# Performance work log

Hardware: AMD Instinct MI355X
Metric: run time of the kernel (lower is better)

Reference implementation:

```python
import jax, jax.numpy as jnp
import numpy as np

K = 3
OFFSET_SCALE = 0.25
GN_GROUPS = 8
GN_EPS = 1e-5


def setup_inputs() -> dict:
    key = jax.random.key(0)
    k1, k2, k3 = jax.random.split(key, 3)
    N, C, H, W = 4, 128, 96, 96
    Cout = 128
    x = jax.random.normal(k1, (N, C, H, W), dtype=jnp.float32)
    # offset head: small random weights so offsets are modest (tanh tames anyway)
    w_head = jax.random.normal(k2, (3, C, 3, 3), dtype=jnp.float32) * 0.05
    b_head = jnp.zeros((3,), dtype=jnp.float32)
    # kaiming-ish scale for the deform conv weight: sqrt(2 / fan_out)
    w_dcn = jax.random.normal(k3, (Cout, C, 3, 3), dtype=jnp.float32) * np.sqrt(2.0 / (Cout * 9))
    gn_gamma = jnp.ones((Cout,), dtype=jnp.float32)
    gn_beta = jnp.zeros((Cout,), dtype=jnp.float32)
    return {"x": x, "w_head": w_head, "b_head": b_head, "w_dcn": w_dcn,
            "gn_gamma": gn_gamma, "gn_beta": gn_beta}


def _conv3x3(x, w, b):
    y = jax.lax.conv_general_dilated(
        x, w, window_strides=(1, 1), padding=((1, 1), (1, 1)),
        dimension_numbers=("NCHW", "OIHW", "NCHW"))
    return y + b[None, :, None, None]


def _deform_sample(xn, py, px):
    # xn: (C,H,W); py/px: (9,H,W) absolute sampling coords (y=row, x=col)
    C, H, W = xn.shape
    y0 = jnp.floor(py).astype(jnp.int32)
    x0 = jnp.floor(px).astype(jnp.int32)
    fy = py - y0
    fx = px - x0
    xf = xn.reshape(C, H * W)

    def corner(yi, xi, wgt):
        valid = (yi >= 0) & (yi < H) & (xi >= 0) & (xi < W)
        idx = jnp.clip(yi, 0, H - 1) * W + jnp.clip(xi, 0, W - 1)  # (9,H,W)
        v = xf[:, idx.reshape(-1)].reshape(C, *idx.shape)  # (C,9,H,W)
        return v * (wgt * valid)[None]

    return (corner(y0, x0, (1 - fy) * (1 - fx))
            + corner(y0, x0 + 1, (1 - fy) * fx)
            + corner(y0 + 1, x0, fy * (1 - fx))
            + corner(y0 + 1, x0 + 1, fy * fx))


def reference(x, w_head, b_head, w_dcn, gn_gamma, gn_beta):
    N, C, H, W = x.shape
    Cout = w_dcn.shape[0]
    stride, pad, dil = 1, 1, 1

    head = _conv3x3(x, w_head, b_head)                 # (N,3,H,W)
    dx, dy, m = head[:, :1], head[:, 1:2], head[:, 2:3]
    mask = jax.nn.sigmoid(m)                           # (N,1,H,W) broadcast over 9 taps
    dx = OFFSET_SCALE * jnp.tanh(dx)
    dy = OFFSET_SCALE * jnp.tanh(dy)

    # serpentine 18-channel offsets, mmcv layout: (oy, ox) pairs per kernel tap
    z = jnp.zeros_like(dx)
    offs = jnp.concatenate(
        [z, z, z, dy, z, -dy, dx, z, z, z, -dx, z, dx, dy, dx, -dy, -dx, dy], axis=1)
    offs = offs.reshape(N, 9, 2, H, W)
    oy, ox = offs[:, :, 0], offs[:, :, 1]              # (N,9,H,W)

    ky = jnp.arange(9) // 3
    kx = jnp.arange(9) % 3
    base_y = (jnp.arange(H) * stride - pad)[None, :, None] + (ky * dil)[:, None, None]
    base_x = (jnp.arange(W) * stride - pad)[None, None, :] + (kx * dil)[:, None, None]
    py = base_y[None] + oy                             # (N,9,H,W)
    px = base_x[None] + ox

    sampled = jax.vmap(_deform_sample)(x, py, px)      # (N,C,9,H,W)
    sampled = sampled * mask[:, None]                  # modulated

    y = jnp.einsum('nckhw,ock->nohw', sampled, w_dcn.reshape(Cout, C, 9))

    # GroupNorm(8, Cout) + ReLU
    G = min(GN_GROUPS, Cout)
    yg = y.reshape(N, G, Cout // G, H, W)
    mu = yg.mean(axis=(2, 3, 4), keepdims=True)
    var = yg.var(axis=(2, 3, 4), keepdims=True)
    yn = ((yg - mu) * jax.lax.rsqrt(var + GN_EPS)).reshape(N, Cout, H, W)
    yn = yn * gn_gamma[None, :, None, None] + gn_beta[None, :, None, None]
    return jax.nn.relu(yn)
```

## Files before the change

kernel.cpp:

```cpp
#include <hip/hip_runtime.h>
#include <hip/hip_bf16.h>
#include <math.h>

#define NB   4
#define CIN  128
#define HH   96
#define WW   96
#define HWN  (HH*WW)
#define NHW  (NB*HWN)
#define COUT 128
#define KW   9
#define KDIM (CIN*KW)
#define GSZ  16
#define PXB  32
#define NBLK (NHW/PXB)
#define XPB  64

typedef __attribute__((ext_vector_type(8))) short bf16x8;
typedef __attribute__((ext_vector_type(4))) float f32x4;

#define OFF_WAH   0
#define OFF_DX    147456
#define OFF_DY    184320
#define OFF_MASK  221184
#define OFF_GN    258048
#define OFF_MAP   258240
#define OFF_PAIR  258496
#define OFF_XT    258560

#define HEADB 1152

__device__ __forceinline__ ushort f2bf(float f) {
    union { float f; uint u; } v; v.f = f;
    uint r = v.u + 0x7fffu + ((v.u >> 16) & 1u);
    return (ushort)(r >> 16);
}

__device__ __forceinline__ void barrier_keep_vm() {
    asm volatile("s_waitcnt lgkmcnt(0)\n\ts_barrier" ::: "memory");
}

__global__ __launch_bounds__(256) void pre_kernel(const float* __restrict__ x,
                                                  const float* __restrict__ w_head,
                                                  const float* __restrict__ b_head,
                                                  const float* __restrict__ wd,
                                                  ushort* __restrict__ wah,
                                                  float* __restrict__ dxv,
                                                  float* __restrict__ dyv,
                                                  float* __restrict__ maskv,
                                                  float* __restrict__ gn_part,
                                                  int* __restrict__ map,
                                                  int* __restrict__ pairB) {
    __shared__ float wl[CIN * 28];
    __shared__ float sp[32][8][13];
    const int b = blockIdx.x, t = threadIdx.x;

    if (b >= HEADB) {
        const int bb = b - HEADB;
        int i = bb * 256 + t;
        {
            int e  = i & 7;
            int l  = (i >> 3) & 63;
            int ot = (i >> 9) & 7;
            int q  = (i >> 12) & 3;
            int k  = i >> 14;
            int o  = ot * 16 + (l & 15);
            int c  = q * 32 + (l >> 4) * 8 + e;
            wah[i] = f2bf(wd[o * KDIM + c * KW + k]);
        }
        if (bb == 0 && t < 128) gn_part[t] = 0.f;
        if (bb == 0 && t < 64) {
            int l = t;
            bf16x8 A1 = {}, B1 = {}, A2 = {}, B2 = {};
            if ((l >> 4) == 0) {
                A1[0] = (short)f2bf((float)((l & 15) + 1));
                B1[0] = (short)f2bf(1.0f);
                A2[0] = (short)f2bf(1.0f);
                B2[0] = (short)f2bf((float)((l & 15) + 1));
            }
            f32x4 d1 = {0.f,0.f,0.f,0.f}, d2 = {0.f,0.f,0.f,0.f};
            d1 = __builtin_amdgcn_mfma_f32_16x16x32_bf16(A1, B1, d1, 0, 0, 0);
            d2 = __builtin_amdgcn_mfma_f32_16x16x32_bf16(A2, B2, d2, 0, 0, 0);
#pragma unroll
            for (int r = 0; r < 4; ++r) {
                int m = (int)(d1[r] + 0.5f) - 1;
                int n = (int)(d2[r] + 0.5f) - 1;
                map[l * 4 + r] = (m << 4) | n;
            }
        }
        if (bb == 1 && t < 64) {
            int l = t;
            union { bf16x8 v; short a[8]; } B;
#pragma unroll
            for (int e = 0; e < 8; ++e) {
                float val = (float)(1u << (((l >> 4) * 8 + e) & 31));
                B.a[e] = (short)f2bf(val);
            }
#pragma unroll
            for (int s = 0; s < 32; ++s) {
                union { bf16x8 v; short a[8]; } A;
#pragma unroll
                for (int e = 0; e < 8; ++e) A.a[e] = 0;
                if ((l >> 4) == (s >> 3)) A.a[s & 7] = (short)f2bf(1.0f);
                f32x4 d = {0.f, 0.f, 0.f, 0.f};
                d = __builtin_amdgcn_mfma_f32_16x16x32_bf16(A.v, B.v, d, 0, 0, 0);
                float v0 = d[0];
                if (l == 0 && v0 > 0.f) {
                    int ex; frexpf(v0, &ex);
                    int j = ex - 1;
                    if (j >= 0 && j < 32) pairB[j] = s;
                }
            }
        }
        return;
    }

    for (int i = t; i < 3456; i += 256) {
        int j = i / KDIM, r = i - j * KDIM;
        int c = r / 9, kk = r - c * 9;
        wl[c * 28 + kk * 3 + j] = w_head[i];
    }
    __syncthreads();

    const int sl = t & 7;
    const int cg = t >> 3;
    const int p0 = b * 32 + sl * 4;
    const int n  = p0 / HWN;
    const int hw = p0 - n * HWN;
    const int h  = hw / WW;
    const int w0 = hw - h * WW;
    const float* xn = x + (size_t)n * CIN * HWN;
    const bool lok = (w0 > 0);
    const bool rok = (w0 < WW - 4);

    float acc[12];
#pragma unroll
    for (int i = 0; i < 12; ++i) acc[i] = 0.f;

#pragma unroll
    for (int cc = 0; cc < 4; ++cc) {
        const int c = cg * 4 + cc;
        const float* xc = xn + (size_t)c * HWN;
        float v[3][6];
#pragma unroll
        for (int r = 0; r < 3; ++r) {
            int y = h - 1 + r;
            if (y >= 0 && y < HH) {
                const float* xr = xc + y * WW + w0;
                float4 m4 = *(const float4*)xr;
                v[r][1] = m4.x; v[r][2] = m4.y; v[r][3] = m4.z; v[r][4] = m4.w;
                v[r][0] = lok ? xr[-1] : 0.f;
                v[r][5] = rok ? xr[4]  : 0.f;
            } else {
#pragma unroll
                for (int i = 0; i < 6; ++i) v[r][i] = 0.f;
            }
        }
        float wr[28];
        const float* wc = &wl[c * 28];
#pragma unroll
        for (int i2 = 0; i2 < 7; ++i2) {
            float4 q4 = *(const float4*)(wc + i2 * 4);
            wr[i2 * 4 + 0] = q4.x; wr[i2 * 4 + 1] = q4.y;
            wr[i2 * 4 + 2] = q4.z; wr[i2 * 4 + 3] = q4.w;
        }
#pragma unroll
        for (int ky = 0; ky < 3; ++ky)
#pragma unroll
            for (int kx = 0; kx < 3; ++kx) {
                const int kk = ky * 3 + kx;
                const float wj0 = wr[kk * 3 + 0];
                const float wj1 = wr[kk * 3 + 1];
                const float wj2 = wr[kk * 3 + 2];
#pragma unroll
                for (int q = 0; q < 4; ++q) {
                    float val = v[ky][q + kx];
                    acc[q * 3 + 0] = fmaf(val, wj0, acc[q * 3 + 0]);
                    acc[q * 3 + 1] = fmaf(val, wj1, acc[q * 3 + 1]);
                    acc[q * 3 + 2] = fmaf(val, wj2, acc[q * 3 + 2]);
                }
            }
    }
#pragma unroll
    for (int i = 0; i < 12; ++i) sp[cg][sl][i] = acc[i];
    __syncthreads();
    if (cg < 8) {
#pragma unroll
        for (int k = 8; k < 32; k += 8)
#pragma unroll
            for (int i = 0; i < 12; ++i) sp[cg][sl][i] += sp[cg + k][sl][i];
    }
    __syncthreads();
    if (t < 32) {
        const int s2 = t >> 2, q = t & 3;
        float b0 = b_head[0], b1 = b_head[1], b2 = b_head[2];
#pragma unroll
        for (int cgi = 0; cgi < 8; ++cgi) {
            b0 += sp[cgi][s2][q * 3 + 0];
            b1 += sp[cgi][s2][q * 3 + 1];
            b2 += sp[cgi][s2][q * 3 + 2];
        }
        int pp = b * 32 + t;
        dxv[pp]   = 0.25f * tanhf(b0);
        dyv[pp]   = 0.25f * tanhf(b1);
        maskv[pp] = 1.f / (1.f + expf(-b2));
    }
}

__global__ __launch_bounds__(256) void xpose_kernel(const float* __restrict__ x,
                                                    const int* __restrict__ pairB,
                                                    float* __restrict__ xt) {
    __shared__ float tile[CIN][XPB + 1];
    __shared__ int sperm[CIN];
    const int b = blockIdx.x, t = threadIdx.x;
    const int p0 = b * XPB;
    const int n  = p0 / HWN, hw0 = p0 % HWN;
    const float* xn = x + (size_t)n * CIN * HWN + hw0;

    if (t < CIN) {
        int q = t >> 5, j = t & 31;
        sperm[t] = q * 32 + (pairB[j] & 31);
    }
    __syncthreads();

#pragma unroll
    for (int rep = 0; rep < 4; ++rep) {
        const int c  = rep * 32 + (t >> 3);
        const int px = (t & 7) * 8;
        const float* src = xn + (size_t)c * HWN + px;
        float4 a = *(const float4*)src;
        float4 bq = *(const float4*)(src + 4);
        tile[c][px + 0] = a.x;  tile[c][px + 1] = a.y;
        tile[c][px + 2] = a.z;  tile[c][px + 3] = a.w;
        tile[c][px + 4] = bq.x; tile[c][px + 5] = bq.y;
        tile[c][px + 6] = bq.z; tile[c][px + 7] = bq.w;
    }
    __syncthreads();

    const int px = t >> 2, jg = t & 3;
    float* dst = xt + ((size_t)p0 + px) * CIN + jg * 32;
#pragma unroll
    for (int jj = 0; jj < 32; jj += 4) {
        float4 v;
        v.x = tile[sperm[jg * 32 + jj + 0]][px];
        v.y = tile[sperm[jg * 32 + jj + 1]][px];
        v.z = tile[sperm[jg * 32 + jj + 2]][px];
        v.w = tile[sperm[jg * 32 + jj + 3]][px];
        *(float4*)(dst + jj) = v;
    }
}

__global__ __launch_bounds__(256) void dcn_kernel(const float* __restrict__ xt,
                                                  const ushort* __restrict__ wah,
                                                  const float* __restrict__ dxv,
                                                  const float* __restrict__ dyv,
                                                  const float* __restrict__ maskv,
                                                  const int* __restrict__ map,
                                                  float* __restrict__ out,
                                                  float* __restrict__ gn_part) {
    __shared__ __attribute__((aligned(16))) ushort sBh[2][4 * PXB * 8];
    __shared__ float sMask[PXB];
    __shared__ float gred[16];

    const int t = threadIdx.x;
    const int lane = t & 63;
    const int wv = t >> 6;
    const int lg = lane >> 4;
    const int ml = lane & 15;
    const int pix = t & 31;
    const int sg  = t >> 5;

    int b = blockIdx.x;
    int nb = (b & 7) * (NBLK / 8) + (b >> 3);
    const int p0  = nb * PXB;
    const int n   = p0 / HWN;
    const int hw0 = p0 % HWN;
    const float* xtn = xt + (size_t)n * HWN * CIN;

    if (t < PXB) sMask[t] = maskv[p0 + t];
    if (t < 16) gred[t] = 0.f;

    const float dxl = dxv[p0 + pix];
    const float dyl = dyv[p0 + pix];
    const int hme = (hw0 + pix) / WW;
    const int wme = (hw0 + pix) % WW;

    f32x4 acc[2][2];
#pragma unroll
    for (int i = 0; i < 2; i++)
#pragma unroll
        for (int j = 0; j < 2; j++) acc[i][j] = (f32x4){0.f, 0.f, 0.f, 0.f};

    const int oyc[9] = {0, 0, 0, 1, 0, -1, 1, 1, -1};
    const int oxc[9] = {0, 1, -1, 0, 0, 0, 1, -1, 1};
    const int ncl[9] = {1, 2, 2, 2, 1, 2, 4, 4, 4};

    int aa[4]; float wq[4];
    float4 vr0, vr1, vr2, vr3;
    bf16x8 An0, An1;

    {
        float py = (float)(hme - 1), px = (float)(wme - 1);
        float fy0 = floorf(py), fx0 = floorf(px);
        int y0 = (int)fy0, x0 = (int)fx0;
        float fy = py - fy0, fx = px - fx0;
#pragma unroll
        for (int j = 0; j < 4; ++j) {
            int yy = y0 + (j >> 1), xx = x0 + (j & 1);
            float wb = ((j >> 1) ? fy : 1.f - fy) * ((j & 1) ? fx : 1.f - fx);
            bool ok = (yy >= 0) && (yy < HH) && (xx >= 0) && (xx < WW);
            aa[j] = min(max(yy, 0), HH - 1) * WW + min(max(xx, 0), WW - 1);
            wq[j] = ok ? wb : 0.f;
        }
        vr0 = *(const float4*)(xtn + ((aa[0] << 7) + sg * 4));
        const size_t abase = (size_t)(wv * 2) * 512 + lane * 8;
        An0 = *(const bf16x8*)(wah + abase);
        An1 = *(const bf16x8*)(wah + abase + 512);
    }

#pragma unroll
    for (int j = 0; j < 36; ++j) {
        const int k = j >> 2;
        const int NC = ncl[k];
        bf16x8 Ah0 = An0, Ah1 = An1;
        union { short4 v; ushort u[4]; } hv;
        {
            float s0 = vr0.x * wq[0], s1 = vr0.y * wq[0];
            float s2 = vr0.z * wq[0], s3 = vr0.w * wq[0];
            if (NC >= 2) {
                s0 = fmaf(vr1.x, wq[1], s0); s1 = fmaf(vr1.y, wq[1], s1);
                s2 = fmaf(vr1.z, wq[1], s2); s3 = fmaf(vr1.w, wq[1], s3);
            }
            if (NC == 4) {
                s0 = fmaf(vr2.x, wq[2], s0); s1 = fmaf(vr2.y, wq[2], s1);
                s2 = fmaf(vr2.z, wq[2], s2); s3 = fmaf(vr2.w, wq[2], s3);
                s0 = fmaf(vr3.x, wq[3], s0); s1 = fmaf(vr3.y, wq[3], s1);
                s2 = fmaf(vr3.z, wq[3], s2); s3 = fmaf(vr3.w, wq[3], s3);
            }
            hv.u[0] = f2bf(s0); hv.u[1] = f2bf(s1);
            hv.u[2] = f2bf(s2); hv.u[3] = f2bf(s3);
        }
        const int wbase = ((sg >> 1) * PXB + pix) * 8 + (sg & 1) * 4;
        *(short4*)&sBh[j & 1][wbase] = hv.v;
        if (j < 35) {
            const int jn = j + 1, kn = jn >> 2, qn = jn & 3;
            if (qn == 0) {
                const int ky = kn / 3, kx = kn - ky * 3;
                float py = (float)(hme - 1 + ky) + (float)oyc[kn] * dxl;
                float px = (float)(wme - 1 + kx) + (float)oxc[kn] * dyl;
                float fy0 = floorf(py), fx0 = floorf(px);
                int y0 = (int)fy0, x0 = (int)fx0;
                float fy = py - fy0, fx = px - fx0;
#pragma unroll
                for (int jj = 0; jj < 4; ++jj) {
                    int yy = y0 + (jj >> 1), xx = x0 + (jj & 1);
                    float wb = ((jj >> 1) ? fy : 1.f - fy) * ((jj & 1) ? fx : 1.f - fx);
                    bool ok = (yy >= 0) && (yy < HH) && (xx >= 0) && (xx < WW);
                    aa[jj] = min(max(yy, 0), HH - 1) * WW + min(max(xx, 0), WW - 1);
                    wq[jj] = ok ? wb : 0.f;
                }
                if (ncl[kn] == 2 && oxc[kn] == 0) { aa[1] = aa[2]; wq[1] = wq[2]; }
            }
            const int NCn = ncl[kn];
            const int co = qn * 32 + sg * 4;
            vr0 = *(const float4*)(xtn + ((aa[0] << 7) + co));
            if (NCn >= 2) vr1 = *(const float4*)(xtn + ((aa[1] << 7) + co));
            if (NCn == 4) {
                vr2 = *(const float4*)(xtn + ((aa[2] << 7) + co));
                vr3 = *(const float4*)(xtn + ((aa[3] << 7) + co));
            }
            const size_t abase = (size_t)((kn * 4 + qn) * 8 + wv * 2) * 512 + lane * 8;
            An0 = *(const bf16x8*)(wah + abase);
            An1 = *(const bf16x8*)(wah + abase + 512);
        }
        barrier_keep_vm();
#pragma unroll
        for (int pt = 0; pt < 2; ++pt) {
            const int rbase = (lg * PXB + pt * 16 + ml) * 8;
            bf16x8 Bh = *(const bf16x8*)&sBh[j & 1][rbase];
            acc[0][pt] = __builtin_amdgcn_mfma_f32_16x16x32_bf16(Ah0, Bh, acc[0][pt], 0, 0, 0);
            acc[1][pt] = __builtin_amdgcn_mfma_f32_16x16x32_bf16(Ah1, Bh, acc[1][pt], 0, 0, 0);
        }
    }

    int4 mn4 = *(const int4*)&map[lane * 4];
    int mn[4] = {mn4.x, mn4.y, mn4.z, mn4.w};
    float s1g[2] = {0.f, 0.f}, s2g[2] = {0.f, 0.f};
#pragma unroll
    for (int ot = 0; ot < 2; ++ot) {
        int otile = wv * 32 + ot * 16;
#pragma unroll
        for (int pt = 0; pt < 2; ++pt) {
#pragma unroll
            for (int r = 0; r < 4; ++r) {
                int m = mn[r] >> 4, nn2 = mn[r] & 15;
                int p = pt * 16 + nn2;
                float v = acc[ot][pt][r] * sMask[p];
                s1g[ot] += v;
                s2g[ot] += v * v;
                out[((size_t)n * COUT + otile + m) * HWN + hw0 + p] = v;
            }
        }
    }
#pragma unroll
    for (int ot = 0; ot < 2; ++ot) {
        int g = wv * 2 + ot;
        atomicAdd(&gred[g * 2 + 0], s1g[ot]);
        atomicAdd(&gred[g * 2 + 1], s2g[ot]);
    }
    __syncthreads();
    if (t < 8) {
        atomicAdd(&gn_part[n * 8 + t],      gred[t * 2 + 0]);
        atomicAdd(&gn_part[64 + n * 8 + t], gred[t * 2 + 1]);
    }
}

__global__ __launch_bounds__(256) void gn_apply(float* __restrict__ out,
                                                const float* __restrict__ gn_part,
                                                const float* __restrict__ gamma,
                                                const float* __restrict__ beta) {
    int i4 = blockIdx.x * 256 + threadIdx.x;
    size_t e = (size_t)i4 * 4;
    int og = (int)(e / HWN);
    int n = og >> 7, o = og & 127;
    int s = n * 8 + (o >> 4);
    const float cnt = (float)GSZ * (float)HWN;
    float s1 = gn_part[s], s2 = gn_part[64 + s];
    float mu = s1 / cnt;
    float var = s2 / cnt - mu * mu;
    float inv = rsqrtf(var + 1e-5f);
    float ga = gamma[o] * inv;
    float be = beta[o] - mu * ga;
    float4 v = *(float4*)(out + e);
    v.x = fmaxf(fmaf(v.x, ga, be), 0.f);
    v.y = fmaxf(fmaf(v.y, ga, be), 0.f);
    v.z = fmaxf(fmaf(v.z, ga, be), 0.f);
    v.w = fmaxf(fmaf(v.w, ga, be), 0.f);
    *(float4*)(out + e) = v;
}

extern "C" void kernel_launch(void* const* d_in, const int* in_sizes, int n_in,
                              void* d_out, int out_size, void* d_ws, size_t ws_size,
                              hipStream_t stream) {
    const float* x       = (const float*)d_in[0];
    const float* w_head  = (const float*)d_in[1];
    const float* b_head  = (const float*)d_in[2];
    const float* w_dcn   = (const float*)d_in[3];
    const float* gamma   = (const float*)d_in[4];
    const float* beta    = (const float*)d_in[5];
    float* out = (float*)d_out;
    float* ws  = (float*)d_ws;

    ushort* wah    = (ushort*)(ws + OFF_WAH);
    float* dxv     = ws + OFF_DX;
    float* dyv     = ws + OFF_DY;
    float* maskv   = ws + OFF_MASK;
    float* gn_part = ws + OFF_GN;
    int*   map     = (int*)(ws + OFF_MAP);
    int*   pairB   = (int*)(ws + OFF_PAIR);
    float* xt      = ws + OFF_XT;

    pre_kernel<<<HEADB + 576, 256, 0, stream>>>(x, w_head, b_head, w_dcn, wah,
                                                dxv, dyv, maskv, gn_part, map, pairB);
    xpose_kernel<<<NHW / XPB, 256, 0, stream>>>(x, pairB, xt);
    dcn_kernel<<<NBLK, 256, 0, stream>>>(xt, wah, dxv, dyv, maskv, map, out, gn_part);
    gn_apply<<<(NB * COUT * HWN) / 4 / 256, 256, 0, stream>>>(out, gn_part, gamma, beta);
}
```

Before: 194.3 us.

## Fuse transpose kernel into pre-kernel and remap dcn thread-to-pixel layout

Folds the x transpose/permute work into the pre_kernel launch as extra blocks, each of which recomputes the MFMA lane permutation locally instead of reading pairB from global memory. This removes one kernel launch and the dependency on pairB between kernels. Shared memory becomes one union buffer sized for the largest role. It also changes the transpose store pattern to row-contiguous float4 writes and swaps the pixel/subgroup thread mapping in dcn_kernel. That mapping swap changes how sampled x rows are gathered and could affect coalescing either way.

```diff
diff --git a/kernel.cpp b/kernel.cpp
--- a/kernel.cpp
+++ b/kernel.cpp
@@ -15,6 +15,7 @@
 #define PXB  32
 #define NBLK (NHW/PXB)
 #define XPB  64
+#define XPOB (NHW/XPB)
 
 typedef __attribute__((ext_vector_type(8))) short bf16x8;
 typedef __attribute__((ext_vector_type(4))) float f32x4;
@@ -50,10 +51,76 @@
                                                   float* __restrict__ maskv,
                                                   float* __restrict__ gn_part,
                                                   int* __restrict__ map,
-                                                  int* __restrict__ pairB) {
-    __shared__ float wl[CIN * 28];
-    __shared__ float sp[32][8][13];
+                                                  int* __restrict__ pairB,
+                                                  float* __restrict__ xt) {
+    __shared__ __attribute__((aligned(16))) float smem[8480];
     const int b = blockIdx.x, t = threadIdx.x;
+
+    if (b >= HEADB + 576) {
+        float (*tile)[XPB + 1] = (float (*)[XPB + 1])smem;
+        int* sperm = (int*)(smem + CIN * (XPB + 1));
+        int* spair = (int*)(smem + CIN * (XPB + 1) + CIN);
+        const int bb2 = b - (HEADB + 576);
+        const int p0 = bb2 * XPB;
+        const int n  = p0 / HWN, hw0 = p0 % HWN;
+        const float* xn = x + (size_t)n * CIN * HWN + hw0;
+
+        if (t < 64) {
+            int l = t;
+            union { bf16x8 v; short a[8]; } B;
+#pragma unroll
+            for (int e = 0; e < 8; ++e) {
+                float val = (float)(1u << (((l >> 4) * 8 + e) & 31));
+                B.a[e] = (short)f2bf(val);
+            }
+#pragma unroll
+            for (int s = 0; s < 32; ++s) {
+                union { bf16x8 v; short a[8]; } A;
+#pragma unroll
+                for (int e = 0; e < 8; ++e) A.a[e] = 0;
+                if ((l >> 4) == (s >> 3)) A.a[s & 7] = (short)f2bf(1.0f);
+                f32x4 d = {0.f, 0.f, 0.f, 0.f};
+                d = __builtin_amdgcn_mfma_f32_16x16x32_bf16(A.v, B.v, d, 0, 0, 0);
+                float v0 = d[0];
+                if (l == 0 && v0 > 0.f) {
+                    int ex; frexpf(v0, &ex);
+                    int j = ex - 1;
+                    if (j >= 0 && j < 32) spair[j] = s;
+                }
+            }
+        }
+        __syncthreads();
+        if (t < CIN) sperm[t] = (t & ~31) | (spair[t & 31] & 31);
+        __syncthreads();
+
+#pragma unroll
+        for (int rep = 0; rep < 4; ++rep) {
+            const int c  = rep * 32 + (t >> 3);
+            const int px = (t & 7) * 8;
+            const float* src = xn + (size_t)c * HWN + px;
+            float4 a = *(const float4*)src;
+            float4 bq = *(const float4*)(src + 4);
+            tile[c][px + 0] = a.x;  tile[c][px + 1] = a.y;
+            tile[c][px + 2] = a.z;  tile[c][px + 3] = a.w;
+            tile[c][px + 4] = bq.x; tile[c][px + 5] = bq.y;
+            tile[c][px + 6] = bq.z; tile[c][px + 7] = bq.w;
+        }
+        __syncthreads();
+
+#pragma unroll
+        for (int wc = 0; wc < 8; ++wc) {
+            const int idx = wc * 256 + t;
+            const int px  = idx >> 5;
+            const int s4  = idx & 31;
+            float4 v;
+            v.x = tile[sperm[s4 * 4 + 0]][px];
+            v.y = tile[sperm[s4 * 4 + 1]][px];
+            v.z = tile[sperm[s4 * 4 + 2]][px];
+            v.w = tile[sperm[s4 * 4 + 3]][px];
+            *(float4*)(xt + ((size_t)(p0 + px)) * CIN + s4 * 4) = v;
+        }
+        return;
+    }
 
     if (b >= HEADB) {
         const int bb = b - HEADB;
@@ -115,6 +182,8 @@
         return;
     }
 
+    float* wl = smem;
+    float (*sp)[8][13] = (float (*)[8][13])(smem + CIN * 28);
     for (int i = t; i < 3456; i += 256) {
         int j = i / KDIM, r = i - j * KDIM;
         int c = r / 9, kk = r - c * 9;
@@ -204,49 +273,6 @@
         dxv[pp]   = 0.25f * tanhf(b0);
         dyv[pp]   = 0.25f * tanhf(b1);
         maskv[pp] = 1.f / (1.f + expf(-b2));
-    }
-}
-
-__global__ __launch_bounds__(256) void xpose_kernel(const float* __restrict__ x,
-                                                    const int* __restrict__ pairB,
-                                                    float* __restrict__ xt) {
-    __shared__ float tile[CIN][XPB + 1];
-    __shared__ int sperm[CIN];
-    const int b = blockIdx.x, t = threadIdx.x;
-    const int p0 = b * XPB;
-    const int n  = p0 / HWN, hw0 = p0 % HWN;
-    const float* xn = x + (size_t)n * CIN * HWN + hw0;
-
-    if (t < CIN) {
-        int q = t >> 5, j = t & 31;
-        sperm[t] = q * 32 + (pairB[j] & 31);
-    }
-    __syncthreads();
-
-#pragma unroll
-    for (int rep = 0; rep < 4; ++rep) {
-        const int c  = rep * 32 + (t >> 3);
-        const int px = (t & 7) * 8;
-        const float* src = xn + (size_t)c * HWN + px;
-        float4 a = *(const float4*)src;
-        float4 bq = *(const float4*)(src + 4);
-        tile[c][px + 0] = a.x;  tile[c][px + 1] = a.y;
-        tile[c][px + 2] = a.z;  tile[c][px + 3] = a.w;
-        tile[c][px + 4] = bq.x; tile[c][px + 5] = bq.y;
-        tile[c][px + 6] = bq.z; tile[c][px + 7] = bq.w;
-    }
-    __syncthreads();
-
-    const int px = t >> 2, jg = t & 3;
-    float* dst = xt + ((size_t)p0 + px) * CIN + jg * 32;
-#pragma unroll
-    for (int jj = 0; jj < 32; jj += 4) {
-        float4 v;
-        v.x = tile[sperm[jg * 32 + jj + 0]][px];
-        v.y = tile[sperm[jg * 32 + jj + 1]][px];
-        v.z = tile[sperm[jg * 32 + jj + 2]][px];
-        v.w = tile[sperm[jg * 32 + jj + 3]][px];
-        *(float4*)(dst + jj) = v;
     }
 }
 
@@ -267,8 +293,8 @@
     const int wv = t >> 6;
     const int lg = lane >> 4;
     const int ml = lane & 15;
-    const int pix = t & 31;
-    const int sg  = t >> 5;
+    const int pix = t >> 3;
+    const int sg  = t & 7;
 
     int b = blockIdx.x;
     int nb = (b & 7) * (NBLK / 8) + (b >> 3);
@@ -460,9 +486,8 @@
     int*   pairB   = (int*)(ws + OFF_PAIR);
     float* xt      = ws + OFF_XT;
 
-    pre_kernel<<<HEADB + 576, 256, 0, stream>>>(x, w_head, b_head, w_dcn, wah,
-                                                dxv, dyv, maskv, gn_part, map, pairB);
-    xpose_kernel<<<NHW / XPB, 256, 0, stream>>>(x, pairB, xt);
+    pre_kernel<<<HEADB + 576 + XPOB, 256, 0, stream>>>(x, w_head, b_head, w_dcn, wah,
+                                                       dxv, dyv, maskv, gn_part, map, pairB, xt);
     dcn_kernel<<<NBLK, 256, 0, stream>>>(xt, wah, dxv, dyv, maskv, map, out, gn_part);
     gn_apply<<<(NB * COUT * HWN) / 4 / 256, 256, 0, stream>>>(out, gn_part, gamma, beta);
 }
```

New measurement: 159.6 us. -17.9%, faster.
